# Performance work log

Hardware: AMD Instinct MI355X
Metric: run time of the kernel (lower is better)

## Reference

```python
import jax, jax.numpy as jnp
import numpy as np

D_MODEL = 64
B, H, S, D = 1, 8, 4096, 64


def setup_inputs() -> dict:
    key = jax.random.key(0)
    k1, k2, k3, k4, k5, k6 = jax.random.split(key, 6)
    Q = jax.random.normal(k1, (B, H, S, D), dtype=jnp.float32)
    K = jax.random.normal(k2, (B, H, S, D), dtype=jnp.float32)
    V = jax.random.normal(k3, (B, H, S, D), dtype=jnp.float32)
    distance_matrix = jax.random.uniform(k4, (B, S, S), dtype=jnp.float32)
    energy_matrix = jax.random.uniform(k5, (B, S, S), dtype=jnp.float32)
    mask = jax.random.randint(k6, (B, 1, S, S), 0, 2, dtype=jnp.int32)
    return {"Q": Q, "K": K, "V": V, "distance_matrix": distance_matrix,
            "energy_matrix": energy_matrix, "mask": mask}


def reference(Q, K, V, distance_matrix, energy_matrix, mask):
    # scores: [B, H, S, S]
    scale = 1.0 / np.sqrt(D_MODEL * 2).astype(np.float32)
    scores = jnp.einsum('bhqd,bhkd->bhqk', Q, K) * scale
    scores = jnp.where(mask == 0, jnp.float32(-1e9), scores)
    attn = jax.nn.softmax(scores, axis=-1)
    context = jnp.einsum('bhqk,bhkd->bhqd', attn, V)
    return context
```

## Files before the change

kernel.cpp:

```cpp
#include <hip/hip_runtime.h>
#include <hip/hip_bf16.h>
#include <stdint.h>

#define S_LEN 4096
#define DH    64
#define NHEAD 8
#define QBLK  64
#define KVBLK 64
#define NKT   (S_LEN / KVBLK)
#define NWRD  (S_LEN / 64)

typedef __attribute__((ext_vector_type(8))) short   short8;
typedef __attribute__((ext_vector_type(8))) unsigned short ushort8;
typedef __attribute__((ext_vector_type(4))) float   f32x4;

#define SCALE 0.08838834764831845f

__device__ __forceinline__ unsigned short f2bf(float x) {
  union { __hip_bfloat16 b; unsigned short u; } v;
  v.b = __float2bfloat16(x);
  return v.u;
}

__device__ __forceinline__ f32x4 mfma16(short8 a, short8 b, f32x4 c) {
  return __builtin_amdgcn_mfma_f32_16x16x32_bf16(a, b, c, 0, 0, 0);
}

__global__ __launch_bounds__(256) void mask_pack_kernel(const int* __restrict__ mask,
                                                        unsigned long long* __restrict__ bits) {
  const int idx = blockIdx.x * 256 + threadIdx.x;
  const unsigned long long b = __ballot(mask[idx] != 0);
  if ((threadIdx.x & 63) == 0) bits[idx >> 6] = b;
}

template <bool PACKED>
__global__ __launch_bounds__(256, 2) void attn_kernel(
    const float* __restrict__ Q, const float* __restrict__ K, const float* __restrict__ V,
    const unsigned long long* __restrict__ bits, const int* __restrict__ maskp,
    float* __restrict__ out) {

  __shared__ __attribute__((aligned(16))) unsigned short Klds[KVBLK * DH];
  __shared__ __attribute__((aligned(16))) unsigned short Vtlds[DH * KVBLK];
  __shared__ __attribute__((aligned(16))) unsigned short Plds[4][16 * KVBLK];
  __shared__ unsigned long long Mlds[QBLK];

  const int tid  = threadIdx.x;
  const int wv   = tid >> 6;
  const int lane = tid & 63;
  const int m    = lane & 15;
  const int g    = lane >> 4;

  const int h  = blockIdx.x >> 6;
  const int qt = blockIdx.x & 63;

  const size_t headoff = (size_t)h * S_LEN * DH;

  short8 aQ[2];
  {
    const float* qp = Q + headoff + (size_t)(qt * QBLK + wv * 16 + m) * DH + g * 8;
#pragma unroll
    for (int c = 0; c < 2; ++c) {
      const float4 f0 = *(const float4*)(qp + c * 32);
      const float4 f1 = *(const float4*)(qp + c * 32 + 4);
      ushort8 u;
      u[0] = f2bf(f0.x * SCALE); u[1] = f2bf(f0.y * SCALE);
      u[2] = f2bf(f0.z * SCALE); u[3] = f2bf(f0.w * SCALE);
      u[4] = f2bf(f1.x * SCALE); u[5] = f2bf(f1.y * SCALE);
      u[6] = f2bf(f1.z * SCALE); u[7] = f2bf(f1.w * SCALE);
      aQ[c] = __builtin_bit_cast(short8, u);
    }
  }

  const int srow = tid >> 2;
  const int sseg = tid & 3;
  const float* kgbase = K + headoff + sseg * 16;
  const float* vgbase = V + headoff + sseg * 16;

  char* const kb = (char*)Klds;
  char* const vb = (char*)Vtlds;
  char* const pb = (char*)(&Plds[wv][0]);

  float4 kreg[4], vreg[4];
  unsigned long long mreg = 0;

  f32x4 acc[4] = {f32x4{0.f,0.f,0.f,0.f}, f32x4{0.f,0.f,0.f,0.f},
                  f32x4{0.f,0.f,0.f,0.f}, f32x4{0.f,0.f,0.f,0.f}};
  float mrun[4] = {-1e9f, -1e9f, -1e9f, -1e9f};
  float lrun[4] = {0.f, 0.f, 0.f, 0.f};

  auto prefetch = [&](int kt) {
    const float* kp = kgbase + (size_t)(kt * KVBLK + srow) * DH;
    const float* vp = vgbase + (size_t)(kt * KVBLK + srow) * DH;
#pragma unroll
    for (int i = 0; i < 4; ++i) kreg[i] = ((const float4*)kp)[i];
#pragma unroll
    for (int i = 0; i < 4; ++i) vreg[i] = ((const float4*)vp)[i];
    if (tid < QBLK) {
      if (PACKED) {
        mreg = bits[(size_t)(qt * QBLK + tid) * NWRD + kt];
      } else {
        const int* mp = maskp + (size_t)(qt * QBLK + tid) * S_LEN + kt * KVBLK;
        unsigned long long bm = 0;
#pragma unroll
        for (int i = 0; i < 16; ++i) {
          const int4 v = ((const int4*)mp)[i];
          const unsigned long long n =
              (unsigned long long)((v.x != 0) | ((v.y != 0) << 1) |
                                   ((v.z != 0) << 2) | ((v.w != 0) << 3));
          bm |= n << (4 * i);
        }
        mreg = bm;
      }
    }
  };

  auto store_stage = [&]() {
    {
      const int swz = (srow & 7) << 4;
      const int b0 = (srow * 128 + sseg * 32) ^ swz;
      const int b1 = (srow * 128 + sseg * 32 + 16) ^ swz;
      ushort8 w0, w1;
      w0[0] = f2bf(kreg[0].x); w0[1] = f2bf(kreg[0].y);
      w0[2] = f2bf(kreg[0].z); w0[3] = f2bf(kreg[0].w);
      w0[4] = f2bf(kreg[1].x); w0[5] = f2bf(kreg[1].y);
      w0[6] = f2bf(kreg[1].z); w0[7] = f2bf(kreg[1].w);
      w1[0] = f2bf(kreg[2].x); w1[1] = f2bf(kreg[2].y);
      w1[2] = f2bf(kreg[2].z); w1[3] = f2bf(kreg[2].w);
      w1[4] = f2bf(kreg[3].x); w1[5] = f2bf(kreg[3].y);
      w1[6] = f2bf(kreg[3].z); w1[7] = f2bf(kreg[3].w);
      *(ushort8*)(kb + b0) = w0;
      *(ushort8*)(kb + b1) = w1;
    }
#pragma unroll
    for (int i = 0; i < 4; ++i) {
      const float4 f = vreg[i];
      const float vals[4] = {f.x, f.y, f.z, f.w};
      const int d0 = sseg * 16 + i * 4;
#pragma unroll
      for (int e = 0; e < 4; ++e) {
        const int d = d0 + e;
        *(unsigned short*)(vb + ((d * 128 + srow * 2) ^ ((d & 7) << 4))) = f2bf(vals[e]);
      }
    }
    if (tid < QBLK) Mlds[tid] = mreg;
  };

  auto compute = [&](int kt) {
    (void)kt;
    f32x4 s[4];
#pragma unroll
    for (int t = 0; t < 4; ++t) {
      const int krow = t * 16 + m;
      const int swz = (krow & 7) << 4;
      const ushort8 b0 = *(const ushort8*)(kb + ((krow * 128 + g * 16) ^ swz));
      const ushort8 b1 = *(const ushort8*)(kb + ((krow * 128 + 64 + g * 16) ^ swz));
      f32x4 z = {0.f, 0.f, 0.f, 0.f};
      z = mfma16(aQ[0], __builtin_bit_cast(short8, b0), z);
      z = mfma16(aQ[1], __builtin_bit_cast(short8, b1), z);
      s[t] = z;
    }

    unsigned long long wrd[4];
#pragma unroll
    for (int r = 0; r < 4; ++r) wrd[r] = Mlds[wv * 16 + g * 4 + r];

    float p[4][4];
#pragma unroll
    for (int r = 0; r < 4; ++r) {
#pragma unroll
      for (int t = 0; t < 4; ++t) {
        const bool keep = (wrd[r] >> (t * 16 + m)) & 1ull;
        p[t][r] = keep ? s[t][r] : -1e9f;
      }
      float rm = fmaxf(fmaxf(p[0][r], p[1][r]), fmaxf(p[2][r], p[3][r]));
      rm = fmaxf(rm, __shfl_xor(rm, 1));
      rm = fmaxf(rm, __shfl_xor(rm, 2));
      rm = fmaxf(rm, __shfl_xor(rm, 4));
      rm = fmaxf(rm, __shfl_xor(rm, 8));
      const float mnew = fmaxf(mrun[r], rm);
      const float sf = __expf(mrun[r] - mnew);
      mrun[r] = mnew;
      float ls = 0.f;
#pragma unroll
      for (int t = 0; t < 4; ++t) {
        const float pe = __expf(p[t][r] - mnew);
        p[t][r] = pe;
        ls += pe;
      }
      lrun[r] = lrun[r] * sf + ls;
#pragma unroll
      for (int t = 0; t < 4; ++t) acc[t][r] *= sf;
    }

#pragma unroll
    for (int t = 0; t < 4; ++t)
#pragma unroll
      for (int r = 0; r < 4; ++r) {
        const int prow = g * 4 + r;
        *(unsigned short*)(pb + ((prow * 128 + (t * 16 + m) * 2) ^ ((prow & 7) << 4))) =
            f2bf(p[t][r]);
      }

    short8 pa[2];
#pragma unroll
    for (int c = 0; c < 2; ++c)
      pa[c] = __builtin_bit_cast(
          short8, *(const ushort8*)(pb + ((m * 128 + c * 64 + g * 16) ^ ((m & 7) << 4))));

#pragma unroll
    for (int c = 0; c < 2; ++c)
#pragma unroll
      for (int t = 0; t < 4; ++t) {
        const int drow = t * 16 + m;
        const ushort8 bv =
            *(const ushort8*)(vb + ((drow * 128 + c * 64 + g * 16) ^ ((drow & 7) << 4)));
        acc[t] = mfma16(pa[c], __builtin_bit_cast(short8, bv), acc[t]);
      }
  };

  prefetch(0);
  store_stage();
  __syncthreads();

  for (int kt = 0; kt < NKT; ++kt) {
    if (kt + 1 < NKT) prefetch(kt + 1);
    compute(kt);
    if (kt + 1 < NKT) {
      __syncthreads();
      store_stage();
      __syncthreads();
    }
  }

  float* op = out + headoff + (size_t)(qt * QBLK + wv * 16) * DH;
#pragma unroll
  for (int r = 0; r < 4; ++r) {
    float ls = lrun[r];
    ls += __shfl_xor(ls, 1);
    ls += __shfl_xor(ls, 2);
    ls += __shfl_xor(ls, 4);
    ls += __shfl_xor(ls, 8);
    const float inv = 1.0f / ls;
#pragma unroll
    for (int t = 0; t < 4; ++t)
      op[(g * 4 + r) * DH + t * 16 + m] = acc[t][r] * inv;
  }
}

extern "C" void kernel_launch(void* const* d_in, const int* in_sizes, int n_in,
                              void* d_out, int out_size, void* d_ws, size_t ws_size,
                              hipStream_t stream) {
  (void)in_sizes; (void)n_in; (void)out_size;
  const float* Q = (const float*)d_in[0];
  const float* K = (const float*)d_in[1];
  const float* V = (const float*)d_in[2];
  const int* mask = (const int*)d_in[5];
  float* out = (float*)d_out;

  const size_t bits_bytes = (size_t)S_LEN * NWRD * sizeof(unsigned long long);
  if (ws_size >= bits_bytes) {
    unsigned long long* bits = (unsigned long long*)d_ws;
    mask_pack_kernel<<<(S_LEN * S_LEN) / 256, 256, 0, stream>>>(mask, bits);
    attn_kernel<true><<<NHEAD * (S_LEN / QBLK), 256, 0, stream>>>(Q, K, V, bits, nullptr, out);
  } else {
    attn_kernel<false><<<NHEAD * (S_LEN / QBLK), 256, 0, stream>>>(Q, K, V, nullptr, mask, out);
  }
}
```

Baseline: 343.0 us.

## Pre-convert Q/K/V to bf16 and double-buffer K/V tiles via direct global-to-LDS loads

Adds pre-pass kernels that convert Q (scaled), K (pre-swizzled) and a transposed V to bf16 in workspace. The attention kernel then streams K/V tiles straight into double-buffered LDS using global_load_lds, replacing per-block fp32 loads, conversions and a two-barrier store stage. The mask packer also processes 32 chunks per thread. This halves K/V reread bandwidth across the 64 query tiles and removes redundant conversion work, at the cost of extra kernel launches, more workspace and doubled LDS use, which may lower occupancy.

```diff
diff --git a/kernel.cpp b/kernel.cpp
--- a/kernel.cpp
+++ b/kernel.cpp
@@ -13,11 +13,13 @@
 typedef __attribute__((ext_vector_type(8))) short   short8;
 typedef __attribute__((ext_vector_type(8))) unsigned short ushort8;
 typedef __attribute__((ext_vector_type(4))) float   f32x4;
+typedef unsigned long long u64;
+typedef unsigned short u16;
 
 #define SCALE 0.08838834764831845f
 
-__device__ __forceinline__ unsigned short f2bf(float x) {
-  union { __hip_bfloat16 b; unsigned short u; } v;
+__device__ __forceinline__ u16 f2bf(float x) {
+  union { __hip_bfloat16 b; u16 u; } v;
   v.b = __float2bfloat16(x);
   return v.u;
 }
@@ -26,23 +28,90 @@
   return __builtin_amdgcn_mfma_f32_16x16x32_bf16(a, b, c, 0, 0, 0);
 }
 
-__global__ __launch_bounds__(256) void mask_pack_kernel(const int* __restrict__ mask,
-                                                        unsigned long long* __restrict__ bits) {
-  const int idx = blockIdx.x * 256 + threadIdx.x;
-  const unsigned long long b = __ballot(mask[idx] != 0);
-  if ((threadIdx.x & 63) == 0) bits[idx >> 6] = b;
-}
-
-template <bool PACKED>
-__global__ __launch_bounds__(256, 2) void attn_kernel(
-    const float* __restrict__ Q, const float* __restrict__ K, const float* __restrict__ V,
-    const unsigned long long* __restrict__ bits, const int* __restrict__ maskp,
+__device__ __forceinline__ void gload_lds16(const void* gsrc, void* ldst) {
+  __builtin_amdgcn_global_load_lds(
+      (const __attribute__((address_space(1))) unsigned int*)gsrc,
+      (__attribute__((address_space(3))) unsigned int*)ldst, 16, 0, 0);
+}
+
+__global__ __launch_bounds__(256) void mask_pack(const int* __restrict__ mask,
+                                                 u64* __restrict__ bits) {
+  size_t idx = (size_t)blockIdx.x * 256 + threadIdx.x;
+  const bool l0 = (threadIdx.x & 63) == 0;
+#pragma unroll
+  for (int i = 0; i < 32; ++i) {
+    const u64 b = __ballot(mask[idx] != 0);
+    if (l0) bits[idx >> 6] = b;
+    idx += (size_t)2048 * 256;
+  }
+}
+
+__global__ __launch_bounds__(256) void conv_qk(const float* __restrict__ Q,
+                                               const float* __restrict__ K,
+                                               u16* __restrict__ Qb,
+                                               u16* __restrict__ Kb) {
+  int cid = blockIdx.x * 256 + threadIdx.x;
+  const int NCH = NHEAD * S_LEN * DH / 8;
+  const bool isK = cid >= NCH;
+  if (isK) cid -= NCH;
+  const int r = cid >> 3, c = cid & 7;
+  if (!isK) {
+    const float* s = Q + (size_t)r * DH + c * 8;
+    const float4 f0 = ((const float4*)s)[0], f1 = ((const float4*)s)[1];
+    ushort8 o;
+    o[0] = f2bf(f0.x * SCALE); o[1] = f2bf(f0.y * SCALE);
+    o[2] = f2bf(f0.z * SCALE); o[3] = f2bf(f0.w * SCALE);
+    o[4] = f2bf(f1.x * SCALE); o[5] = f2bf(f1.y * SCALE);
+    o[6] = f2bf(f1.z * SCALE); o[7] = f2bf(f1.w * SCALE);
+    *(ushort8*)(Qb + (size_t)r * DH + c * 8) = o;
+  } else {
+    const int cs = c ^ (r & 7);
+    const float* s = K + (size_t)r * DH + cs * 8;
+    const float4 f0 = ((const float4*)s)[0], f1 = ((const float4*)s)[1];
+    ushort8 o;
+    o[0] = f2bf(f0.x); o[1] = f2bf(f0.y); o[2] = f2bf(f0.z); o[3] = f2bf(f0.w);
+    o[4] = f2bf(f1.x); o[5] = f2bf(f1.y); o[6] = f2bf(f1.z); o[7] = f2bf(f1.w);
+    *(ushort8*)(Kb + (size_t)r * DH + c * 8) = o;
+  }
+}
+
+__global__ __launch_bounds__(256) void conv_v(const float* __restrict__ V,
+                                              u16* __restrict__ Vtb) {
+  __shared__ u16 T[64][72];
+  const int h = blockIdx.x >> 6, st = blockIdx.x & 63;
+  const int r = threadIdx.x >> 2, cs4 = (threadIdx.x & 3) * 16;
+  const float* src = V + ((size_t)(h * S_LEN) + st * 64 + r) * DH + cs4;
+#pragma unroll
+  for (int i = 0; i < 4; ++i) {
+    const float4 f = ((const float4*)src)[i];
+    T[cs4 + i * 4 + 0][r] = f2bf(f.x);
+    T[cs4 + i * 4 + 1][r] = f2bf(f.y);
+    T[cs4 + i * 4 + 2][r] = f2bf(f.z);
+    T[cs4 + i * 4 + 3][r] = f2bf(f.w);
+  }
+  __syncthreads();
+  const int d = threadIdx.x >> 2;
+  u16* orow = Vtb + ((size_t)(h * DH + d)) * S_LEN + st * 64;
+#pragma unroll
+  for (int cc = 0; cc < 2; ++cc) {
+    const int c = cc * 4 + (threadIdx.x & 3);
+    const int cs = c ^ (d & 7);
+    ushort8 o;
+#pragma unroll
+    for (int j = 0; j < 8; ++j) o[j] = T[d][cs * 8 + j];
+    *(ushort8*)(orow + c * 8) = o;
+  }
+}
+
+__global__ __launch_bounds__(256, 2) void attn2(
+    const u16* __restrict__ Qb, const u16* __restrict__ Kb,
+    const u16* __restrict__ Vtb, const u64* __restrict__ bits,
     float* __restrict__ out) {
 
-  __shared__ __attribute__((aligned(16))) unsigned short Klds[KVBLK * DH];
-  __shared__ __attribute__((aligned(16))) unsigned short Vtlds[DH * KVBLK];
-  __shared__ __attribute__((aligned(16))) unsigned short Plds[4][16 * KVBLK];
-  __shared__ unsigned long long Mlds[QBLK];
+  __shared__ __attribute__((aligned(16))) u16 Kl[2][KVBLK * DH];
+  __shared__ __attribute__((aligned(16))) u16 Vl[2][DH * KVBLK];
+  __shared__ __attribute__((aligned(16))) u16 Pl[4][16 * KVBLK];
+  __shared__ u64 Ml[2][QBLK];
 
   const int tid  = threadIdx.x;
   const int wv   = tid >> 6;
@@ -53,6 +122,154 @@
   const int h  = blockIdx.x >> 6;
   const int qt = blockIdx.x & 63;
 
+  const char* kh = (const char*)Kb  + (size_t)h * S_LEN * DH * 2;
+  const char* vh = (const char*)Vtb + (size_t)h * DH * S_LEN * 2;
+
+  short8 aQ[2];
+  {
+    const u16* qp = Qb + (size_t)h * S_LEN * DH +
+                    (size_t)(qt * QBLK + wv * 16 + m) * DH + g * 8;
+    aQ[0] = __builtin_bit_cast(short8, *(const ushort8*)(qp));
+    aQ[1] = __builtin_bit_cast(short8, *(const ushort8*)(qp + 32));
+  }
+
+  char* const pb = (char*)&Pl[wv][0];
+
+  f32x4 acc[4] = {f32x4{0.f,0.f,0.f,0.f}, f32x4{0.f,0.f,0.f,0.f},
+                  f32x4{0.f,0.f,0.f,0.f}, f32x4{0.f,0.f,0.f,0.f}};
+  float mrun[4] = {-1e9f, -1e9f, -1e9f, -1e9f};
+  float lrun[4] = {0.f, 0.f, 0.f, 0.f};
+
+  const int o0  = wv * 2048 + lane * 16;
+  const int vd0 = wv * 16 + (lane >> 3);
+  const int vb  = (lane & 7) * 16;
+
+  auto stage = [&](int kt, int nb) {
+    const char* ks = kh + (size_t)kt * 8192 + o0;
+    char* kd = (char*)&Kl[nb][0] + wv * 2048;
+    gload_lds16(ks, kd);
+    gload_lds16(ks + 1024, kd + 1024);
+    const char* vs = vh + (size_t)vd0 * (S_LEN * 2) + (size_t)kt * 128 + vb;
+    char* vd = (char*)&Vl[nb][0] + wv * 2048;
+    gload_lds16(vs, vd);
+    gload_lds16(vs + (size_t)8 * (S_LEN * 2), vd + 1024);
+    if (tid < QBLK) Ml[nb][tid] = bits[(size_t)(qt * QBLK + tid) * NWRD + kt];
+  };
+
+  auto compute = [&](int cur) {
+    const char* kb = (const char*)&Kl[cur][0];
+    const char* vbp = (const char*)&Vl[cur][0];
+
+    f32x4 s[4];
+#pragma unroll
+    for (int t = 0; t < 4; ++t) {
+      const int krow = t * 16 + m;
+      const int swz = (krow & 7) << 4;
+      const ushort8 b0 = *(const ushort8*)(kb + ((krow * 128 + g * 16) ^ swz));
+      const ushort8 b1 = *(const ushort8*)(kb + ((krow * 128 + 64 + g * 16) ^ swz));
+      f32x4 z = {0.f, 0.f, 0.f, 0.f};
+      z = mfma16(aQ[0], __builtin_bit_cast(short8, b0), z);
+      z = mfma16(aQ[1], __builtin_bit_cast(short8, b1), z);
+      s[t] = z;
+    }
+
+    u64 wrd[4];
+#pragma unroll
+    for (int r = 0; r < 4; ++r) wrd[r] = Ml[cur][wv * 16 + g * 4 + r];
+
+    float p[4][4];
+#pragma unroll
+    for (int r = 0; r < 4; ++r) {
+#pragma unroll
+      for (int t = 0; t < 4; ++t) {
+        const bool keep = (wrd[r] >> (t * 16 + m)) & 1ull;
+        p[t][r] = keep ? s[t][r] : -1e9f;
+      }
+      float rm = fmaxf(fmaxf(p[0][r], p[1][r]), fmaxf(p[2][r], p[3][r]));
+      rm = fmaxf(rm, __shfl_xor(rm, 1));
+      rm = fmaxf(rm, __shfl_xor(rm, 2));
+      rm = fmaxf(rm, __shfl_xor(rm, 4));
+      rm = fmaxf(rm, __shfl_xor(rm, 8));
+      const float mnew = fmaxf(mrun[r], rm);
+      const float sf = __expf(mrun[r] - mnew);
+      mrun[r] = mnew;
+      float ls = 0.f;
+#pragma unroll
+      for (int t = 0; t < 4; ++t) {
+        const float pe = __expf(p[t][r] - mnew);
+        p[t][r] = pe;
+        ls += pe;
+      }
+      lrun[r] = lrun[r] * sf + ls;
+#pragma unroll
+      for (int t = 0; t < 4; ++t) acc[t][r] *= sf;
+    }
+
+#pragma unroll
+    for (int t = 0; t < 4; ++t)
+#pragma unroll
+      for (int r = 0; r < 4; ++r) {
+        const int prow = g * 4 + r;
+        *(u16*)(pb + ((prow * 128 + (t * 16 + m) * 2) ^ ((prow & 7) << 4))) =
+            f2bf(p[t][r]);
+      }
+
+    short8 pa[2];
+#pragma unroll
+    for (int c = 0; c < 2; ++c)
+      pa[c] = __builtin_bit_cast(
+          short8, *(const ushort8*)(pb + ((m * 128 + c * 64 + g * 16) ^ ((m & 7) << 4))));
+
+#pragma unroll
+    for (int c = 0; c < 2; ++c)
+#pragma unroll
+      for (int t = 0; t < 4; ++t) {
+        const int drow = t * 16 + m;
+        const ushort8 bv =
+            *(const ushort8*)(vbp + ((drow * 128 + c * 64 + g * 16) ^ ((drow & 7) << 4)));
+        acc[t] = mfma16(pa[c], __builtin_bit_cast(short8, bv), acc[t]);
+      }
+  };
+
+  stage(0, 0);
+  __syncthreads();
+  int cur = 0;
+  for (int kt = 0; kt < NKT; ++kt) {
+    if (kt + 1 < NKT) stage(kt + 1, cur ^ 1);
+    compute(cur);
+    __syncthreads();
+    cur ^= 1;
+  }
+
+  float* op = out + (size_t)h * S_LEN * DH + (size_t)(qt * QBLK + wv * 16) * DH;
+#pragma unroll
+  for (int r = 0; r < 4; ++r) {
+    float ls = lrun[r];
+    ls += __shfl_xor(ls, 1);
+    ls += __shfl_xor(ls, 2);
+    ls += __shfl_xor(ls, 4);
+    ls += __shfl_xor(ls, 8);
+    const float inv = 1.0f / ls;
+#pragma unroll
+    for (int t = 0; t < 4; ++t)
+      op[(g * 4 + r) * DH + t * 16 + m] = acc[t][r] * inv;
+  }
+}
+
+template <bool PACKED>
+__global__ __launch_bounds__(256, 2) void attn_fb(
+    const float* __restrict__ Q, const float* __restrict__ K, const float* __restrict__ V,
+    const u64* __restrict__ bits, const int* __restrict__ maskp,
+    float* __restrict__ out) {
+
+  __shared__ __attribute__((aligned(16))) u16 Klds[KVBLK * DH];
+  __shared__ __attribute__((aligned(16))) u16 Vtlds[DH * KVBLK];
+  __shared__ __attribute__((aligned(16))) u16 Plds[4][16 * KVBLK];
+  __shared__ u64 Mlds[QBLK];
+
+  const int tid = threadIdx.x, wv = tid >> 6, lane = tid & 63;
+  const int m = lane & 15, g = lane >> 4;
+  const int h = blockIdx.x >> 6, qt = blockIdx.x & 63;
   const size_t headoff = (size_t)h * S_LEN * DH;
 
   short8 aQ[2];
@@ -71,18 +288,15 @@
     }
   }
 
-  const int srow = tid >> 2;
-  const int sseg = tid & 3;
+  const int srow = tid >> 2, sseg = tid & 3;
   const float* kgbase = K + headoff + sseg * 16;
   const float* vgbase = V + headoff + sseg * 16;
-
   char* const kb = (char*)Klds;
   char* const vb = (char*)Vtlds;
   char* const pb = (char*)(&Plds[wv][0]);
 
   float4 kreg[4], vreg[4];
-  unsigned long long mreg = 0;
-
+  u64 mreg = 0;
   f32x4 acc[4] = {f32x4{0.f,0.f,0.f,0.f}, f32x4{0.f,0.f,0.f,0.f},
                   f32x4{0.f,0.f,0.f,0.f}, f32x4{0.f,0.f,0.f,0.f}};
   float mrun[4] = {-1e9f, -1e9f, -1e9f, -1e9f};
@@ -100,13 +314,12 @@
         mreg = bits[(size_t)(qt * QBLK + tid) * NWRD + kt];
       } else {
         const int* mp = maskp + (size_t)(qt * QBLK + tid) * S_LEN + kt * KVBLK;
-        unsigned long long bm = 0;
+        u64 bm = 0;
 #pragma unroll
         for (int i = 0; i < 16; ++i) {
           const int4 v = ((const int4*)mp)[i];
-          const unsigned long long n =
-              (unsigned long long)((v.x != 0) | ((v.y != 0) << 1) |
-                                   ((v.z != 0) << 2) | ((v.w != 0) << 3));
+          const u64 n = (u64)((v.x != 0) | ((v.y != 0) << 1) |
+                              ((v.z != 0) << 2) | ((v.w != 0) << 3));
           bm |= n << (4 * i);
         }
         mreg = bm;
@@ -139,14 +352,13 @@
 #pragma unroll
       for (int e = 0; e < 4; ++e) {
         const int d = d0 + e;
-        *(unsigned short*)(vb + ((d * 128 + srow * 2) ^ ((d & 7) << 4))) = f2bf(vals[e]);
+        *(u16*)(vb + ((d * 128 + srow * 2) ^ ((d & 7) << 4))) = f2bf(vals[e]);
       }
     }
     if (tid < QBLK) Mlds[tid] = mreg;
   };
 
-  auto compute = [&](int kt) {
-    (void)kt;
+  auto compute = [&]() {
     f32x4 s[4];
 #pragma unroll
     for (int t = 0; t < 4; ++t) {
@@ -159,11 +371,9 @@
       z = mfma16(aQ[1], __builtin_bit_cast(short8, b1), z);
       s[t] = z;
     }
-
-    unsigned long long wrd[4];
+    u64 wrd[4];
 #pragma unroll
     for (int r = 0; r < 4; ++r) wrd[r] = Mlds[wv * 16 + g * 4 + r];
-
     float p[4][4];
 #pragma unroll
     for (int r = 0; r < 4; ++r) {
@@ -191,22 +401,19 @@
 #pragma unroll
       for (int t = 0; t < 4; ++t) acc[t][r] *= sf;
     }
-
 #pragma unroll
     for (int t = 0; t < 4; ++t)
 #pragma unroll
       for (int r = 0; r < 4; ++r) {
         const int prow = g * 4 + r;
-        *(unsigned short*)(pb + ((prow * 128 + (t * 16 + m) * 2) ^ ((prow & 7) << 4))) =
+        *(u16*)(pb + ((prow * 128 + (t * 16 + m) * 2) ^ ((prow & 7) << 4))) =
             f2bf(p[t][r]);
       }
-
     short8 pa[2];
 #pragma unroll
     for (int c = 0; c < 2; ++c)
       pa[c] = __builtin_bit_cast(
           short8, *(const ushort8*)(pb + ((m * 128 + c * 64 + g * 16) ^ ((m & 7) << 4))));
-
 #pragma unroll
     for (int c = 0; c < 2; ++c)
 #pragma unroll
@@ -221,10 +428,9 @@
   prefetch(0);
   store_stage();
   __syncthreads();
-
   for (int kt = 0; kt < NKT; ++kt) {
     if (kt + 1 < NKT) prefetch(kt + 1);
-    compute(kt);
+    compute();
     if (kt + 1 < NKT) {
       __syncthreads();
       store_stage();
@@ -257,12 +463,24 @@
   const int* mask = (const int*)d_in[5];
   float* out = (float*)d_out;
 
-  const size_t bits_bytes = (size_t)S_LEN * NWRD * sizeof(unsigned long long);
-  if (ws_size >= bits_bytes) {
-    unsigned long long* bits = (unsigned long long*)d_ws;
-    mask_pack_kernel<<<(S_LEN * S_LEN) / 256, 256, 0, stream>>>(mask, bits);
-    attn_kernel<true><<<NHEAD * (S_LEN / QBLK), 256, 0, stream>>>(Q, K, V, bits, nullptr, out);
+  const size_t SZ = (size_t)NHEAD * S_LEN * DH;
+  const size_t bits_b = (size_t)S_LEN * NWRD * 8;
+  const size_t need = bits_b + 3 * SZ * 2;
+
+  if (ws_size >= need) {
+    u64* bits = (u64*)d_ws;
+    u16* Qb  = (u16*)((char*)d_ws + bits_b);
+    u16* Kb  = Qb + SZ;
+    u16* Vtb = Kb + SZ;
+    mask_pack<<<2048, 256, 0, stream>>>(mask, bits);
+    conv_qk<<<2048, 256, 0, stream>>>(Q, K, Qb, Kb);
+    conv_v<<<512, 256, 0, stream>>>(V, Vtb);
+    attn2<<<NHEAD * (S_LEN / QBLK), 256, 0, stream>>>(Qb, Kb, Vtb, bits, out);
+  } else if (ws_size >= bits_b) {
+    u64* bits = (u64*)d_ws;
+    mask_pack<<<2048, 256, 0, stream>>>(mask, bits);
+    attn_fb<true><<<NHEAD * (S_LEN / QBLK), 256, 0, stream>>>(Q, K, V, bits, nullptr, out);
   } else {
-    attn_kernel<false><<<NHEAD * (S_LEN / QBLK), 256, 0, stream>>>(Q, K, V, nullptr, mask, out);
-  }
-}
+    attn_fb<false><<<NHEAD * (S_LEN / QBLK), 256, 0, stream>>>(Q, K, V, nullptr, mask, out);
+  }
+}
```

After: 312.5 us. -8.9%, faster.
